# Kernel optimization log

Measured on AMD Instinct MI355X. Metric: run time of the kernel, lower is better.

The kernel has to match this reference:

```python
import jax, jax.numpy as jnp
import numpy as np

K = 3            # kernel_size
PAD = 1
DIL = 1
STRIDE = 1
G = 4            # group
OFFSET_SCALE = 1.0


def _grid_sample_bilinear(img, grid):
    # img: (B, C, Hi, Wi); grid: (B, L, P, 2) normalized to [-1,1] (x,y order)
    # mode='bilinear', padding_mode='zeros', align_corners=False
    B, C, Hi, Wi = img.shape
    gx = (grid[..., 0] + 1.0) * (Wi * 0.5) - 0.5   # (B, L, P)
    gy = (grid[..., 1] + 1.0) * (Hi * 0.5) - 0.5
    x0 = jnp.floor(gx)
    y0 = jnp.floor(gy)
    wx = gx - x0                                   # frac weights
    wy = gy - y0
    x0i = x0.astype(jnp.int32)
    y0i = y0.astype(jnp.int32)
    img_flat = img.reshape(B, C, Hi * Wi)

    def gather(xi, yi):
        valid = (xi >= 0) & (xi < Wi) & (yi >= 0) & (yi < Hi)
        xi_c = jnp.clip(xi, 0, Wi - 1)
        yi_c = jnp.clip(yi, 0, Hi - 1)
        idx = (yi_c * Wi + xi_c).reshape(B, -1)    # (B, L*P)
        vals = jax.vmap(lambda im, ix: im[:, ix])(img_flat, idx)   # (B, C, L*P)
        vals = vals.reshape(B, C, xi.shape[1], xi.shape[2])
        return vals * valid[:, None].astype(img.dtype)

    v00 = gather(x0i, y0i)
    v01 = gather(x0i + 1, y0i)
    v10 = gather(x0i, y0i + 1)
    v11 = gather(x0i + 1, y0i + 1)
    wx = wx[:, None]
    wy = wy[:, None]
    return (v00 * (1 - wx) * (1 - wy) + v01 * wx * (1 - wy)
            + v10 * (1 - wx) * wy + v11 * wx * wy)   # (B, C, L, P)


def reference(img1, kernel_v, kernel_h, offset, weight):
    N, C, H, W = img1.shape
    gc = C // G
    P = K * K
    # separable per-pixel kernel: (N,G*K,H,W) x (N,K,H,W) -> (N,G*K*K,H,W)
    kernel = jnp.einsum('bcij,bdij->bcdij', kernel_h, kernel_v).reshape(N, G * P, H, W)

    x = jnp.transpose(img1, (0, 2, 3, 1))             # NHWC
    mask = jnp.transpose(weight, (0, 2, 3, 1))        # (N,H,W,G*P)
    off = jnp.transpose(offset, (0, 2, 3, 1))         # (N,H,W,G*P*2)
    ker = jnp.transpose(kernel, (0, 2, 3, 1))         # (N,H,W,G*P)

    x = jnp.pad(x, ((0, 0), (PAD, PAD), (PAD, PAD), (0, 0)))
    Hi, Wi = H + 2 * PAD, W + 2 * PAD
    Ho = (Hi - (DIL * (K - 1) + 1)) // STRIDE + 1
    Wo = (Wi - (DIL * (K - 1) + 1)) // STRIDE + 1

    # reference points (normalized, x-y order)
    ry = (DIL * (K - 1) // 2 + 0.5 + jnp.arange(Ho, dtype=jnp.float32) * STRIDE) / Hi
    rx = (DIL * (K - 1) // 2 + 0.5 + jnp.arange(Wo, dtype=jnp.float32) * STRIDE) / Wi
    ref = jnp.stack(jnp.broadcast_arrays(rx[None, :], ry[:, None]), axis=-1)  # (Ho,Wo,2)

    # dilation grid: torch meshgrid('ij') over (kw,kh) -> x varies along axis 0
    base = jnp.linspace(-(DIL * (K - 1) // 2),
                        -(DIL * (K - 1) // 2) + (K - 1) * DIL, K, dtype=jnp.float32)
    gxk = jnp.broadcast_to(base[:, None], (K, K)) / Wi
    gyk = jnp.broadcast_to(base[None, :], (K, K)) / Hi
    dgrid = jnp.stack([gxk, gyk], -1).reshape(P, 2)
    dgrid = jnp.tile(dgrid[None], (G, 1, 1)).reshape(G * P, 2)   # (G*P,2)

    loc = ref[None, :, :, None, :] + dgrid[None, None, None] * OFFSET_SCALE  # (1,Ho,Wo,G*P,2)
    loc = loc.reshape(1, Ho, Wo, G * P * 2)
    norm = jnp.tile(jnp.array([Wi, Hi], dtype=jnp.float32), G * P)
    loc = loc + off * OFFSET_SCALE / norm                       # (N,Ho,Wo,G*P*2)

    grids = 2.0 * loc - 1.0
    grids = grids.reshape(N, Ho * Wo, G, P, 2).transpose(0, 2, 1, 3, 4)
    grids = grids.reshape(N * G, Ho * Wo, P, 2)

    inp = x.reshape(N, Hi * Wi, G * gc).transpose(0, 2, 1).reshape(N * G, gc, Hi, Wi)
    sampled = _grid_sample_bilinear(inp, grids)                 # (N*G, gc, Ho*Wo, P)

    mask_r = mask.reshape(N, Ho * Wo, G, P).transpose(0, 2, 1, 3).reshape(N * G, 1, Ho * Wo, P)
    ker_r = ker.reshape(N, Ho * Wo, G, P).transpose(0, 2, 1, 3).reshape(N * G, 1, Ho * Wo, P)

    out = (sampled * mask_r * ker_r).sum(-1)                    # (N*G, gc, Ho*Wo)
    out = out.reshape(N, G * gc, Ho * Wo).transpose(0, 2, 1).reshape(N, Ho, Wo, C)
    return jnp.transpose(out, (0, 3, 1, 2))                     # NCHW


def setup_inputs() -> dict:
    key = jax.random.key(0)
    k1, k2, k3, k4, k5 = jax.random.split(key, 5)
    N, C, H, W = 2, 64, 256, 256
    P = K * K
    return {
        'img1': jax.random.normal(k1, (N, C, H, W), dtype=jnp.float32),
        'kernel_v': jax.random.normal(k2, (N, K, H, W), dtype=jnp.float32),
        'kernel_h': jax.random.normal(k3, (N, G * K, H, W), dtype=jnp.float32),
        'offset': jax.random.normal(k4, (N, G * P * 2, H, W), dtype=jnp.float32),
        'weight': jax.random.normal(k5, (N, G * P, H, W), dtype=jnp.float32),
    }
```

## Files before the change

### kernel.cpp

```cpp
#include <hip/hip_runtime.h>
#include <hip/hip_fp16.h>

#define HH 256
#define WW 256
#define HWSZ (HH*WW)
#define CC 64
#define GG 4
#define GC 16
#define KK 3
#define PP 9
#define NB 2
#define NBG (NB*GG)
#define NBLK_RP (NBG*HH)
#define NBLK_MAIN (NBG*1024)

typedef float f32x4 __attribute__((ext_vector_type(4)));

__global__ __launch_bounds__(256) void repack_kernel(
    const float* __restrict__ img, __half* __restrict__ pk)
{
    int bid = blockIdx.x;
    int y  = bid & (HH - 1);
    int bg = bid >> 8;
    int g  = bg & (GG - 1);
    int b  = bg >> 2;
    int x  = threadIdx.x;

    const float* src = img + (size_t)(b*CC + g*GC) * HWSZ + y*WW + x;
    float v[GC];
#pragma unroll
    for (int c = 0; c < GC; ++c) v[c] = src[c*HWSZ];

    __half2 hh[8];
#pragma unroll
    for (int i = 0; i < 8; ++i) hh[i] = __floats2half2_rn(v[2*i], v[2*i+1]);

    uint4* dst = (uint4*)(pk + ((size_t)bg*HWSZ + y*WW + x) * GC);
    dst[0] = *(uint4*)&hh[0];
    dst[1] = *(uint4*)&hh[4];
}

__global__ __launch_bounds__(256, 4) void misc_filter_coop(
    const __half* __restrict__ pk,
    const float* __restrict__ kv,
    const float* __restrict__ kh,
    const float* __restrict__ off,
    const float* __restrict__ wgt,
    float* __restrict__ out)
{
    int phys = blockIdx.x;
    int logical = (phys & 7) * (NBLK_MAIN / 8) + (phys >> 3);
    int bg  = logical >> 10;
    int blk = logical & 1023;
    int g   = bg & (GG - 1);
    int b   = bg >> 2;

    int tx = blk & 15;
    int ty = blk >> 4;
    const int tilebase = ty*4*WW + tx*16;

    int t  = threadIdx.x;

    __shared__ float Wlds[PP][64][4];
    __shared__ int   Olds[PP][64][2];

    const float* offb = off + (size_t)(b*GG*PP*2 + g*PP*2) * HWSZ + tilebase;
    const float* wgtb = wgt + (size_t)(b*GG*PP   + g*PP  ) * HWSZ + tilebase;
    const float* khb  = kh  + (size_t)(b*GG*KK   + g*KK  ) * HWSZ + tilebase;
    const float* kvb  = kv  + (size_t)(b*KK) * HWSZ + tilebase;

    for (int j = t; j < 64*PP; j += 256) {
        int pidx = j & 63;
        int col  = j & 15;
        int row  = (j >> 4) & 3;
        int tap  = j >> 6;
        int kx   = (tap * 11) >> 5;
        int ky   = tap - 3*kx;
        int pixoff = row*WW + col;
        int pixel1 = tilebase + pixoff;
        int yy = pixel1 >> 8;
        int xx = pixel1 & (WW - 1);

        float ox  = offb[(2*tap  )*HWSZ + pixoff];
        float oy  = offb[(2*tap+1)*HWSZ + pixoff];
        float wv  = wgtb[tap*HWSZ + pixoff];
        float khv = khb[kx*HWSZ + pixoff];
        float kvv = kvb[ky*HWSZ + pixoff];
        float wp  = wv * (khv * kvv);

        float ux = (float)(xx + kx - 1) + ox;
        float uy = (float)(yy + ky - 1) + oy;
        float fx = floorf(ux), fy = floorf(uy);
        float wx = ux - fx,    wy = uy - fy;
        int x0 = (int)fx, y0 = (int)fy;
        int x1 = x0 + 1,  y1 = y0 + 1;
        bool vx0 = (unsigned)x0 < (unsigned)WW;
        bool vx1 = (unsigned)x1 < (unsigned)WW;
        bool vy0 = (unsigned)y0 < (unsigned)HH;
        bool vy1 = (unsigned)y1 < (unsigned)HH;

        float ql = vx0 ? (1.f - wx) : (vx1 ? wx : 0.f);
        float qr = (vx0 && vx1) ? wx : 0.f;
        int   xb = vx0 ? x0 : (vx1 ? x1 : 0);
        float wy0 = vy0 ? (1.f - wy) : 0.f;
        float wy1 = vy1 ? wy : 0.f;
        int y0c = min(max(y0, 0), HH-1);
        int y1c = min(max(y1, 0), HH-1);

        *(float4*)&Wlds[tap][pidx][0] = make_float4(wy0*ql*wp, wy0*qr*wp,
                                                    wy1*ql*wp, wy1*qr*wp);
        *(int2*)&Olds[tap][pidx][0]   = make_int2((y0c*WW + xb)*32,
                                                  (y1c*WW + xb)*32);
    }
    __syncthreads();

    int q  = t & 3;
    int pi = t >> 2;
    int pixel = tilebase + (pi >> 4)*WW + (pi & 15);

    const __half* pkb = pk + (size_t)bg * HWSZ * GC;
    const unsigned laneoff = (unsigned)q * 16u;

    float a0=0.f,a1=0.f,a2=0.f,a3=0.f,a4=0.f,a5=0.f,a6=0.f,a7=0.f;
    f32x4  wvb[2];
    int2   ovb[2];
    float  wA[4], wB[4];
    uint4  vv[4][2];

#define GLOAD(dst, boff) \
    asm volatile("global_load_dwordx4 %0, %1, %2" \
                 : "=v"(dst) : "v"(boff), "s"(pkb) : "memory")

#define WAITV(N) do { \
    asm volatile("s_waitcnt vmcnt(" #N ")" ::: "memory"); \
    __builtin_amdgcn_sched_barrier(0); } while (0)

#define LDSPREF(p) do { if ((p) < PP) {                                         \
    wvb[(p)&1] = *(const f32x4*)&Wlds[(p) < PP ? (p) : 0][pi][0];               \
    ovb[(p)&1] = *(const int2*)&Olds[(p) < PP ? (p) : 0][pi][0]; } } while (0)

#define TAP_L(p) do {                                                           \
    const int bi_ = (p) % 4;                                                    \
    f32x4 f_ = wvb[(p)&1];                                                      \
    wA[bi_] = (q & 2) ? f_[1] : f_[0];                                          \
    wB[bi_] = (q & 2) ? f_[3] : f_[2];                                          \
    int2 o_ = ovb[(p)&1];                                                       \
    GLOAD(vv[bi_][0], (unsigned)o_.x + laneoff);                                \
    GLOAD(vv[bi_][1], (unsigned)o_.y + laneoff);                                \
} while (0)

#define FMA8(u_, w_) do {                                                       \
    const __half2* h2_ = (const __half2*)&(u_);                                 \
    float2 f0_ = __half22float2(h2_[0]);                                        \
    float2 f1_ = __half22float2(h2_[1]);                                        \
    float2 f2_ = __half22float2(h2_[2]);                                        \
    float2 f3_ = __half22float2(h2_[3]);                                        \
    a0 = fmaf(f0_.x, (w_), a0); a1 = fmaf(f0_.y, (w_), a1);                     \
    a2 = fmaf(f1_.x, (w_), a2); a3 = fmaf(f1_.y, (w_), a3);                     \
    a4 = fmaf(f2_.x, (w_), a4); a5 = fmaf(f2_.y, (w_), a5);                     \
    a6 = fmaf(f3_.x, (w_), a6); a7 = fmaf(f3_.y, (w_), a7);                     \
} while (0)

#define TAP_FMA(p) do {                                                         \
    const int bi_ = (p) % 4;                                                    \
    FMA8(vv[bi_][0], wA[bi_]);                                                  \
    FMA8(vv[bi_][1], wB[bi_]);                                                  \
} while (0)

    LDSPREF(0);
    LDSPREF(1); TAP_L(0);
    LDSPREF(2); TAP_L(1);
    LDSPREF(3); TAP_L(2);
    LDSPREF(4); TAP_L(3);
    LDSPREF(5); WAITV(6); TAP_FMA(0); TAP_L(4);
    LDSPREF(6); WAITV(6); TAP_FMA(1); TAP_L(5);
    LDSPREF(7); WAITV(6); TAP_FMA(2); TAP_L(6);
    LDSPREF(8); WAITV(6); TAP_FMA(3); TAP_L(7);
                WAITV(6); TAP_FMA(4); TAP_L(8);
    WAITV(6); TAP_FMA(5);
    WAITV(4); TAP_FMA(6);
    WAITV(2); TAP_FMA(7);
    WAITV(0); TAP_FMA(8);

#undef GLOAD
#undef WAITV
#undef LDSPREF
#undef TAP_L
#undef FMA8
#undef TAP_FMA

    a0 += __shfl_xor(a0, 2); a1 += __shfl_xor(a1, 2);
    a2 += __shfl_xor(a2, 2); a3 += __shfl_xor(a3, 2);
    a4 += __shfl_xor(a4, 2); a5 += __shfl_xor(a5, 2);
    a6 += __shfl_xor(a6, 2); a7 += __shfl_xor(a7, 2);

    float* outp = out + (size_t)(b*CC + g*GC + (q&1)*8 + ((q&2)?4:0)) * HWSZ + pixel;
    if (q & 2) {
        outp[0*HWSZ] = a4; outp[1*HWSZ] = a5; outp[2*HWSZ] = a6; outp[3*HWSZ] = a7;
    } else {
        outp[0*HWSZ] = a0; outp[1*HWSZ] = a1; outp[2*HWSZ] = a2; outp[3*HWSZ] = a3;
    }
}

__global__ __launch_bounds__(256) void misc_filter_direct(
    const float* __restrict__ img,
    const float* __restrict__ kv,
    const float* __restrict__ kh,
    const float* __restrict__ off,
    const float* __restrict__ wgt,
    float* __restrict__ out)
{
    int phys = blockIdx.x;
    int logical = (phys & 7) * (NBLK_RP / 8) + (phys >> 3);
    int y  = logical & (HH - 1);
    int bg = logical >> 8;
    int g  = bg & (GG - 1);
    int b  = bg >> 2;
    int x  = threadIdx.x;

    const float* imgp = img + (size_t)(b*CC + g*GC) * HWSZ;
    int pix = y*WW + x;
    const float* offp = off + (size_t)(b*GG*PP*2 + g*PP*2) * HWSZ + pix;
    const float* wgtp = wgt + (size_t)(b*GG*PP   + g*PP  ) * HWSZ + pix;
    const float* khp  = kh  + (size_t)(b*GG*KK   + g*KK  ) * HWSZ + pix;
    const float* kvp  = kv  + (size_t)(b*KK) * HWSZ + pix;

    float khr[KK], kvr[KK];
#pragma unroll
    for (int i = 0; i < KK; ++i) { khr[i] = khp[i*HWSZ]; kvr[i] = kvp[i*HWSZ]; }
    float acc[GC];
#pragma unroll
    for (int c = 0; c < GC; ++c) acc[c] = 0.f;

#pragma unroll
    for (int p = 0; p < PP; ++p) {
        const int kx = p / KK, ky = p % KK;
        float ox = offp[(2*p  )*HWSZ];
        float oy = offp[(2*p+1)*HWSZ];
        float wp = wgtp[p*HWSZ] * khr[kx] * kvr[ky];
        float ux = (float)(x + kx - 1) + ox;
        float uy = (float)(y + ky - 1) + oy;
        float fx = floorf(ux), fy = floorf(uy);
        float wx = ux - fx,    wy = uy - fy;
        int x0 = (int)fx, y0 = (int)fy;
        int x1 = x0 + 1,  y1 = y0 + 1;
        bool vx0 = (unsigned)x0 < (unsigned)WW;
        bool vx1 = (unsigned)x1 < (unsigned)WW;
        bool vy0 = (unsigned)y0 < (unsigned)HH;
        bool vy1 = (unsigned)y1 < (unsigned)HH;
        float w00 = (1.f-wx)*(1.f-wy)*wp; if (!(vx0 && vy0)) w00 = 0.f;
        float w01 =      wx *(1.f-wy)*wp; if (!(vx1 && vy0)) w01 = 0.f;
        float w10 = (1.f-wx)*     wy *wp; if (!(vx0 && vy1)) w10 = 0.f;
        float w11 =      wx *     wy *wp; if (!(vx1 && vy1)) w11 = 0.f;
        int x0c = min(max(x0, 0), WW-1), x1c = min(max(x1, 0), WW-1);
        int y0c = min(max(y0, 0), HH-1), y1c = min(max(y1, 0), HH-1);
        int i00 = y0c*WW + x0c, i01 = y0c*WW + x1c;
        int i10 = y1c*WW + x0c, i11 = y1c*WW + x1c;
#pragma unroll
        for (int c = 0; c < GC; ++c) {
            const float* pl = imgp + c*HWSZ;
            acc[c] = fmaf(w00, pl[i00], acc[c]);
            acc[c] = fmaf(w01, pl[i01], acc[c]);
            acc[c] = fmaf(w10, pl[i10], acc[c]);
            acc[c] = fmaf(w11, pl[i11], acc[c]);
        }
    }
    float* outp = out + (size_t)(b*CC + g*GC) * HWSZ + pix;
#pragma unroll
    for (int c = 0; c < GC; ++c) outp[c*HWSZ] = acc[c];
}

extern "C" void kernel_launch(void* const* d_in, const int* in_sizes, int n_in,
                              void* d_out, int out_size, void* d_ws, size_t ws_size,
                              hipStream_t stream) {
    const float* img = (const float*)d_in[0];
    const float* kv  = (const float*)d_in[1];
    const float* kh  = (const float*)d_in[2];
    const float* off = (const float*)d_in[3];
    const float* wgt = (const float*)d_in[4];
    float* out = (float*)d_out;

    const size_t need = (size_t)NBG * HWSZ * GC * sizeof(__half) + (1u << 20);
    if (ws_size >= need) {
        __half* pkh = (__half*)d_ws;
        repack_kernel<<<dim3(NBLK_RP), dim3(WW), 0, stream>>>(img, pkh);
        misc_filter_coop<<<dim3(NBLK_MAIN), dim3(256), 0, stream>>>(pkh, kv, kh, off, wgt, out);
    } else {
        misc_filter_direct<<<dim3(NBLK_RP), dim3(WW), 0, stream>>>(img, kv, kh, off, wgt, out);
    }
}
```

Before: 43.47 us.

## Stage packed image halo region in LDS and gather bilinear corners from shared memory

Each block now copies a 32x18 halo window of the fp16-packed image, padded 7 pixels around its 16x4 tile, into XOR-swizzled LDS. Sampling offsets that land inside the window are encoded as LDS addresses, and only out-of-window samples fall back to global loads, flagged by the sign bit. The hand-scheduled asynchronous global-load pipeline is replaced by a simple unrolled loop of LDS reads. This is meant to cut repeated global and L2 gather traffic, at the cost of about 18KB of extra LDS per block, which may reduce occupancy, plus a branchy fallback path that runs often because offsets are random normal values.

```diff
diff --git a/kernel.cpp b/kernel.cpp
--- a/kernel.cpp
+++ b/kernel.cpp
@@ -13,6 +13,9 @@
 #define NBG (NB*GG)
 #define NBLK_RP (NBG*HH)
 #define NBLK_MAIN (NBG*1024)
+#define RW 32
+#define RH 18
+#define RC (RW*RH)
 
 typedef float f32x4 __attribute__((ext_vector_type(4)));
 
@@ -58,11 +61,27 @@
     int tx = blk & 15;
     int ty = blk >> 4;
     const int tilebase = ty*4*WW + tx*16;
+    const int rx0 = tx*16 - 7;
+    const int ry0 = ty*4  - 7;
 
     int t  = threadIdx.x;
 
+    __shared__ uint4 stage[RC*2];
     __shared__ float Wlds[PP][64][4];
     __shared__ int   Olds[PP][64][2];
+
+    const __half* pkb = pk + (size_t)bg * HWSZ * GC;
+
+    for (int j = t; j < RC*2; j += 256) {
+        int cell = j >> 1, half = j & 1;
+        int ryc = cell >> 5;
+        int cx  = cell & 31;
+        int gx = min(max(rx0 + cx, 0), WW-1);
+        int gy = min(max(ry0 + ryc, 0), HH-1);
+        const uint4* src = (const uint4*)((const char*)pkb + (gy*WW + gx)*32 + half*16);
+        unsigned saddr = ((unsigned)(cell*32) ^ (((unsigned)ryc & 3u) << 5)) + half*16;
+        *(uint4*)((char*)stage + saddr) = *src;
+    }
 
     const float* offb = off + (size_t)(b*GG*PP*2 + g*PP*2) * HWSZ + tilebase;
     const float* wgtb = wgt + (size_t)(b*GG*PP   + g*PP  ) * HWSZ + tilebase;
@@ -107,10 +126,20 @@
         int y0c = min(max(y0, 0), HH-1);
         int y1c = min(max(y1, 0), HH-1);
 
+        int ix  = xb - rx0;
+        int iy0 = y0c - ry0;
+        int iy1 = y1c - ry0;
+        bool inx = (unsigned)ix < (unsigned)(RW-1);
+        int o0 = (inx && (unsigned)iy0 < (unsigned)RH)
+               ? (((iy0 << 5) + ix) * 32 | (iy0 & 3))
+               : (int)(0x80000000u | (unsigned)((y0c*WW + xb)*32));
+        int o1 = (inx && (unsigned)iy1 < (unsigned)RH)
+               ? (((iy1 << 5) + ix) * 32 | (iy1 & 3))
+               : (int)(0x80000000u | (unsigned)((y1c*WW + xb)*32));
+
         *(float4*)&Wlds[tap][pidx][0] = make_float4(wy0*ql*wp, wy0*qr*wp,
                                                     wy1*ql*wp, wy1*qr*wp);
-        *(int2*)&Olds[tap][pidx][0]   = make_int2((y0c*WW + xb)*32,
-                                                  (y1c*WW + xb)*32);
+        *(int2*)&Olds[tap][pidx][0]   = make_int2(o0, o1);
     }
     __syncthreads();
 
@@ -118,35 +147,19 @@
     int pi = t >> 2;
     int pixel = tilebase + (pi >> 4)*WW + (pi & 15);
 
-    const __half* pkb = pk + (size_t)bg * HWSZ * GC;
-    const unsigned laneoff = (unsigned)q * 16u;
+    const char* sb = (const char*)&stage[0];
+    const char* pg = (const char*)pkb;
+    const unsigned qcell = (unsigned)(q >> 1) * 32u;
+    const unsigned qhalf = (unsigned)(q & 1) * 16u;
 
     float a0=0.f,a1=0.f,a2=0.f,a3=0.f,a4=0.f,a5=0.f,a6=0.f,a7=0.f;
-    f32x4  wvb[2];
-    int2   ovb[2];
-    float  wA[4], wB[4];
-    uint4  vv[4][2];
-
-#define GLOAD(dst, boff) \
-    asm volatile("global_load_dwordx4 %0, %1, %2" \
-                 : "=v"(dst) : "v"(boff), "s"(pkb) : "memory")
-
-#define WAITV(N) do { \
-    asm volatile("s_waitcnt vmcnt(" #N ")" ::: "memory"); \
-    __builtin_amdgcn_sched_barrier(0); } while (0)
-
-#define LDSPREF(p) do { if ((p) < PP) {                                         \
-    wvb[(p)&1] = *(const f32x4*)&Wlds[(p) < PP ? (p) : 0][pi][0];               \
-    ovb[(p)&1] = *(const int2*)&Olds[(p) < PP ? (p) : 0][pi][0]; } } while (0)
-
-#define TAP_L(p) do {                                                           \
-    const int bi_ = (p) % 4;                                                    \
-    f32x4 f_ = wvb[(p)&1];                                                      \
-    wA[bi_] = (q & 2) ? f_[1] : f_[0];                                          \
-    wB[bi_] = (q & 2) ? f_[3] : f_[2];                                          \
-    int2 o_ = ovb[(p)&1];                                                       \
-    GLOAD(vv[bi_][0], (unsigned)o_.x + laneoff);                                \
-    GLOAD(vv[bi_][1], (unsigned)o_.y + laneoff);                                \
+
+#define LDSCORNER(v_, o_) do {                                                  \
+    unsigned base_ = (unsigned)(o_) & ~3u;                                      \
+    unsigned xorv_ = ((unsigned)(o_) & 3u) << 5;                                \
+    v_ = *(const uint4*)(sb + (((base_ + qcell) ^ xorv_) + qhalf));             \
+    if (__builtin_expect((o_) < 0, 0))                                          \
+        v_ = *(const uint4*)(pg + (((o_) & 0x7FFFFFFF) + (unsigned)q*16u));     \
 } while (0)
 
 #define FMA8(u_, w_) do {                                                       \
@@ -161,33 +174,21 @@
     a6 = fmaf(f3_.x, (w_), a6); a7 = fmaf(f3_.y, (w_), a7);                     \
 } while (0)
 
-#define TAP_FMA(p) do {                                                         \
-    const int bi_ = (p) % 4;                                                    \
-    FMA8(vv[bi_][0], wA[bi_]);                                                  \
-    FMA8(vv[bi_][1], wB[bi_]);                                                  \
-} while (0)
-
-    LDSPREF(0);
-    LDSPREF(1); TAP_L(0);
-    LDSPREF(2); TAP_L(1);
-    LDSPREF(3); TAP_L(2);
-    LDSPREF(4); TAP_L(3);
-    LDSPREF(5); WAITV(6); TAP_FMA(0); TAP_L(4);
-    LDSPREF(6); WAITV(6); TAP_FMA(1); TAP_L(5);
-    LDSPREF(7); WAITV(6); TAP_FMA(2); TAP_L(6);
-    LDSPREF(8); WAITV(6); TAP_FMA(3); TAP_L(7);
-                WAITV(6); TAP_FMA(4); TAP_L(8);
-    WAITV(6); TAP_FMA(5);
-    WAITV(4); TAP_FMA(6);
-    WAITV(2); TAP_FMA(7);
-    WAITV(0); TAP_FMA(8);
-
-#undef GLOAD
-#undef WAITV
-#undef LDSPREF
-#undef TAP_L
+#pragma unroll
+    for (int p = 0; p < PP; ++p) {
+        f32x4 f = *(const f32x4*)&Wlds[p][pi][0];
+        int2  o = *(const int2*)&Olds[p][pi][0];
+        float wA = (q & 2) ? f[1] : f[0];
+        float wB = (q & 2) ? f[3] : f[2];
+        uint4 v0, v1;
+        LDSCORNER(v0, o.x);
+        LDSCORNER(v1, o.y);
+        FMA8(v0, wA);
+        FMA8(v1, wB);
+    }
+
+#undef LDSCORNER
 #undef FMA8
-#undef TAP_FMA
 
     a0 += __shfl_xor(a0, 2); a1 += __shfl_xor(a1, 2);
     a2 += __shfl_xor(a2, 2); a3 += __shfl_xor(a3, 2);
```

After: 60.48 us. 39.1% more time.
